# Kernel tuning notes

Measured on AMD Instinct MI355X. Metric: run time of the kernel, lower is better.

## Reference

```python
import jax, jax.numpy as jnp
import numpy as np

B, S, E, H = 2, 2048, 1024, 16
DH = E // H  # 64
FF = 4 * E


def setup_inputs() -> dict:
    key = jax.random.key(0)
    ks = jax.random.split(key, 13)
    s = 0.02
    return {
        "x": jax.random.normal(ks[0], (B, S, E), dtype=jnp.float32),
        "Wq": jax.random.normal(ks[1], (H, E, DH), dtype=jnp.float32) * s,
        "Wk": jax.random.normal(ks[2], (H, E, DH), dtype=jnp.float32) * s,
        "Wv": jax.random.normal(ks[3], (H, E, DH), dtype=jnp.float32) * s,
        "Wo": jax.random.normal(ks[4], (E, E), dtype=jnp.float32) * s,
        "bo": jnp.zeros((E,), dtype=jnp.float32),
        "W1": jax.random.normal(ks[5], (E, FF), dtype=jnp.float32) * s,
        "b1": jnp.zeros((FF,), dtype=jnp.float32),
        "W2": jax.random.normal(ks[6], (FF, E), dtype=jnp.float32) * s,
        "b2": jnp.zeros((E,), dtype=jnp.float32),
        "g1": jnp.ones((E,), dtype=jnp.float32),
        "beta1": jnp.zeros((E,), dtype=jnp.float32),
        "g2": jnp.ones((E,), dtype=jnp.float32),
        "beta2": jnp.zeros((E,), dtype=jnp.float32),
    }


def _layernorm(x, g, b, eps=1e-5):
    mu = jnp.mean(x, axis=-1, keepdims=True)
    var = jnp.var(x, axis=-1, keepdims=True)
    return (x - mu) * jax.lax.rsqrt(var + eps) * g + b


def reference(x, Wq, Wk, Wv, Wo, bo, W1, b1, W2, b2, g1, beta1, g2, beta2):
    # Pre-LN attention (dropout is identity in eval mode)
    nx = _layernorm(x, g1, beta1)
    # per-head projections, batched over heads: [B,H,S,DH]
    q = jnp.einsum('bse,hed->bhsd', nx, Wq)
    k = jnp.einsum('bse,hed->bhsd', nx, Wk)
    v = jnp.einsum('bse,hed->bhsd', nx, Wv)
    scores = jnp.einsum('bhqd,bhkd->bhqk', q, k) * (DH ** -0.5)  # [B,H,S,S]
    seq = x.shape[1]
    causal = jnp.tril(jnp.ones((seq, seq), dtype=bool))
    scores = jnp.where(causal, scores, -jnp.inf)
    w = jax.nn.softmax(scores, axis=-1)
    attn = jnp.einsum('bhqk,bhkd->bhqd', w, v)  # [B,H,S,DH]
    # concat heads (head order matches ModuleList cat order)
    attn = attn.transpose(0, 2, 1, 3).reshape(x.shape[0], seq, E)
    attn_out = attn @ Wo + bo
    x = x + attn_out
    # FFN
    nx2 = _layernorm(x, g2, beta2)
    ffn = jax.nn.relu(nx2 @ W1 + b1) @ W2 + b2
    return x + ffn
```

## Files before the change

### kernel.cpp

```cpp
#include <hip/hip_runtime.h>


typedef __attribute__((ext_vector_type(8))) short short8;
typedef __attribute__((ext_vector_type(4))) float floatx4;

__device__ inline unsigned short f32_to_bf16(float f) {
  unsigned u = __float_as_uint(f);
  unsigned rb = (u >> 16) & 1u;
  u += 0x7fffu + rb;
  return (unsigned short)(u >> 16);
}
__device__ inline unsigned f32_to_bf16_hi(float f) {
  return (__float_as_uint(f) + 0x8000u) >> 16;
}
__device__ inline float bf16_to_f32(unsigned short u) {
  return __uint_as_float(((unsigned)u) << 16);
}

__global__ __launch_bounds__(256) void transpose_to_bf16(
    const float* __restrict__ in, unsigned short* __restrict__ out,
    int R, int C, int ldo, long in_bs, long out_bs) {
  __shared__ float tile[32][33];
  in  += (size_t)blockIdx.z * in_bs;
  out += (size_t)blockIdx.z * out_bs;
  const int c0 = blockIdx.x * 32, r0 = blockIdx.y * 32;
  const int tx = threadIdx.x & 31, ty = threadIdx.x >> 5;
#pragma unroll
  for (int i = 0; i < 32; i += 8)
    tile[ty + i][tx] = in[(size_t)(r0 + ty + i) * C + c0 + tx];
  __syncthreads();
#pragma unroll
  for (int i = 0; i < 32; i += 8)
    out[(size_t)(c0 + ty + i) * ldo + r0 + tx] = f32_to_bf16(tile[tx][ty + i]);
}

__global__ __launch_bounds__(256) void transpose_v(
    const unsigned short* __restrict__ qkv, unsigned short* __restrict__ vT) {
  __shared__ unsigned short tile[32][33];
  const int bh = blockIdx.z, b = bh >> 4, h = bh & 15;
  const int k0 = blockIdx.x * 32, d0 = blockIdx.y * 32;
  const int tx = threadIdx.x & 31, ty = threadIdx.x >> 5;
#pragma unroll
  for (int i = 0; i < 32; i += 8)
    tile[ty + i][tx] = qkv[(size_t)(b * 2048 + k0 + ty + i) * 3072 + 2048 + h * 64 + d0 + tx];
  __syncthreads();
#pragma unroll
  for (int i = 0; i < 32; i += 8)
    vT[((size_t)bh * 64 + d0 + ty + i) * 2048 + k0 + tx] = tile[tx][ty + i];
}

__global__ __launch_bounds__(256) void layernorm_bf16(
    const float* __restrict__ x, const float* __restrict__ g,
    const float* __restrict__ be, unsigned short* __restrict__ out) {
  const int row = blockIdx.x;
  const int t = threadIdx.x;
  floatx4 v = ((const floatx4*)(x + (size_t)row * 1024))[t];
  float s  = v[0] + v[1] + v[2] + v[3];
  float s2 = v[0]*v[0] + v[1]*v[1] + v[2]*v[2] + v[3]*v[3];
#pragma unroll
  for (int off = 1; off < 64; off <<= 1) {
    s  += __shfl_xor(s, off);
    s2 += __shfl_xor(s2, off);
  }
  __shared__ float red[8];
  const int wave = t >> 6, lane = t & 63;
  if (lane == 0) { red[wave] = s; red[wave + 4] = s2; }
  __syncthreads();
  float ts  = red[0] + red[1] + red[2] + red[3];
  float ts2 = red[4] + red[5] + red[6] + red[7];
  float mu  = ts * (1.f / 1024.f);
  float var = ts2 * (1.f / 1024.f) - mu * mu;
  float rs  = rsqrtf(var + 1e-5f);
  floatx4 gv = ((const floatx4*)g)[t];
  floatx4 bv = ((const floatx4*)be)[t];
  ushort4 ov;
  ov.x = f32_to_bf16((v[0] - mu) * rs * gv[0] + bv[0]);
  ov.y = f32_to_bf16((v[1] - mu) * rs * gv[1] + bv[1]);
  ov.z = f32_to_bf16((v[2] - mu) * rs * gv[2] + bv[2]);
  ov.w = f32_to_bf16((v[3] - mu) * rs * gv[3] + bv[3]);
  ((ushort4*)(out + (size_t)row * 1024))[t] = ov;
}

__global__ __launch_bounds__(256, 4) void gemm_bf16(
    const unsigned short* __restrict__ A, const unsigned short* __restrict__ Bt,
    const float* __restrict__ bias, const float* __restrict__ resid,
    void* __restrict__ Cout, int M, int N, int Kfull, int Klen, int mode) {
  __shared__ unsigned short As[2][128 * 36];
  __shared__ unsigned short Bs[2][128 * 36];
  const int t = threadIdx.x;
  const int NB = gridDim.x;
  const int bid = blockIdx.y * NB + blockIdx.x;
  const int xcd = bid & 7, slot = bid >> 3;
  const int m0 = (xcd * 4 + slot / NB) * 128;
  const int n0 = (slot % NB) * 128;
  const int koff = blockIdx.z * Klen;
  const int lane = t & 63, wave = t >> 6;
  const int wm = (wave >> 1) * 64, wn = (wave & 1) * 64;
  const int l15 = lane & 15, quad = lane >> 4;

  floatx4 acc[4][4];
#pragma unroll
  for (int i = 0; i < 4; ++i)
#pragma unroll
    for (int j = 0; j < 4; ++j) acc[i][j] = floatx4{0.f, 0.f, 0.f, 0.f};

  const int srow = t >> 1;
  const int scol = (t & 1) * 16;
  const unsigned short* Ag = A + (size_t)(m0 + srow) * Kfull + koff + scol;
  const unsigned short* Bg = Bt + (size_t)(n0 + srow) * Kfull + koff + scol;
  const int sdst = srow * 36 + scol;

  uint4 pa0 = *(const uint4*)(Ag);
  uint4 pa1 = *(const uint4*)(Ag + 8);
  uint4 pb0 = *(const uint4*)(Bg);
  uint4 pb1 = *(const uint4*)(Bg + 8);

  const int KT = Klen >> 5;
  int buf = 0;
  for (int kt = 0; kt < KT; ++kt) {
    *(uint4*)&As[buf][sdst]     = pa0;
    *(uint4*)&As[buf][sdst + 8] = pa1;
    *(uint4*)&Bs[buf][sdst]     = pb0;
    *(uint4*)&Bs[buf][sdst + 8] = pb1;
    if (kt + 1 < KT) {
      const int ko = (kt + 1) * 32;
      pa0 = *(const uint4*)(Ag + ko);
      pa1 = *(const uint4*)(Ag + ko + 8);
      pb0 = *(const uint4*)(Bg + ko);
      pb1 = *(const uint4*)(Bg + ko + 8);
    }
    __syncthreads();
    short8 a[4], b[4];
#pragma unroll
    for (int i = 0; i < 4; ++i)
      a[i] = *(const short8*)&As[buf][(wm + i * 16 + l15) * 36 + quad * 8];
#pragma unroll
    for (int i = 0; i < 4; ++i)
      b[i] = *(const short8*)&Bs[buf][(wn + i * 16 + l15) * 36 + quad * 8];
#pragma unroll
    for (int i = 0; i < 4; ++i)
#pragma unroll
      for (int j = 0; j < 4; ++j)
        acc[i][j] = __builtin_amdgcn_mfma_f32_16x16x32_bf16(a[i], b[j], acc[i][j], 0, 0, 0);
    buf ^= 1;
  }

  const size_t poff = (size_t)blockIdx.z * 4096 * 1024;
#pragma unroll
  for (int i = 0; i < 4; ++i)
#pragma unroll
    for (int j = 0; j < 4; ++j) {
      const int col = n0 + wn + j * 16 + l15;
      const int rb = m0 + wm + i * 16 + quad * 4;
#pragma unroll
      for (int r = 0; r < 4; ++r) {
        const int row = rb + r;
        float v = acc[i][j][r];
        if (mode == 0) {
          ((unsigned short*)Cout)[(size_t)row * N + col] = f32_to_bf16(v);
        } else if (mode == 1) {
          v += bias[col] + resid[(size_t)row * N + col];
          ((float*)Cout)[(size_t)row * N + col] = v;
        } else if (mode == 2) {
          v += bias[col];
          v = fmaxf(v, 0.f);
          ((unsigned short*)Cout)[(size_t)row * N + col] = f32_to_bf16(v);
        } else {
          ((float*)Cout)[poff + (size_t)row * N + col] = v;
        }
      }
    }
}

__global__ __launch_bounds__(256) void splitk_reduce(
    const float* __restrict__ p, const float* __restrict__ bias,
    const float* __restrict__ resid, float* __restrict__ out) {
  const int t = threadIdx.x;
  const size_t base = (size_t)blockIdx.x * 256 + t;
  floatx4 a = ((const floatx4*)p)[base];
  floatx4 b = ((const floatx4*)p)[1048576 + base];
  floatx4 rv = ((const floatx4*)resid)[base];
  floatx4 bv = ((const floatx4*)bias)[t];
  ((floatx4*)out)[base] = a + b + rv + bv;
}

__global__ __launch_bounds__(256, 3) void flash_attn_mfma(
    const unsigned short* __restrict__ qkv,
    const unsigned short* __restrict__ vT,
    unsigned short* __restrict__ attn) {
  const int b = blockIdx.z, h = blockIdx.y, bh = b * 16 + h;
  const int qt = 15 - (int)blockIdx.x;
  const int q0 = qt * 128;
  const int t = threadIdx.x;
  const int wave = t >> 6, lane = t & 63;
  const int l15 = lane & 15, quad = lane >> 4;

  __shared__ unsigned short Ks[2][64][68];
  __shared__ unsigned short Vs[2][64][68];
  __shared__ unsigned short Ps[4][32][68];

  const size_t qbase = (size_t)b * 2048 * 3072;
  const int qrow_w = q0 + wave * 32;
  const unsigned short* Kbase = qkv + qbase + 1024 + h * 64;
  const unsigned short* Vbase = vT + (size_t)bh * 64 * 2048;

  short8 qf[2][2];
#pragma unroll
  for (int mf = 0; mf < 2; ++mf)
#pragma unroll
    for (int kc = 0; kc < 2; ++kc) {
      short8 raw = *(const short8*)(qkv + qbase +
          (size_t)(qrow_w + mf * 16 + l15) * 3072 + h * 64 + kc * 32 + quad * 8);
      short8 sc;
#pragma unroll
      for (int j = 0; j < 8; ++j)
        sc[j] = (short)f32_to_bf16(bf16_to_f32((unsigned short)raw[j]) * 0.125f);
      qf[mf][kc] = sc;
    }

  floatx4 o[2][4];
  float l_s[2] = {0.f, 0.f};
#pragma unroll
  for (int mf = 0; mf < 2; ++mf)
#pragma unroll
    for (int jd = 0; jd < 4; ++jd) o[mf][jd] = floatx4{0.f, 0.f, 0.f, 0.f};

  const int sr = t >> 3, so = (t & 7) * 8;

  uint4 kr0 = *(const uint4*)(Kbase + (size_t)sr * 3072 + so);
  uint4 kr1 = *(const uint4*)(Kbase + (size_t)(sr + 32) * 3072 + so);
  uint4 vr0 = *(const uint4*)(Vbase + (size_t)sr * 2048 + so);
  uint4 vr1 = *(const uint4*)(Vbase + (size_t)(sr + 32) * 2048 + so);

  const int ntiles = 2 * qt + 2;
  int buf = 0;
  for (int kt = 0; kt < ntiles; ++kt) {
    const int k0 = kt * 64;
    *(uint4*)&Ks[buf][sr][so]      = kr0;
    *(uint4*)&Ks[buf][sr + 32][so] = kr1;
    *(uint4*)&Vs[buf][sr][so]      = vr0;
    *(uint4*)&Vs[buf][sr + 32][so] = vr1;
    if (kt + 1 < ntiles) {
      const int k1 = k0 + 64;
      kr0 = *(const uint4*)(Kbase + (size_t)(k1 + sr) * 3072 + so);
      kr1 = *(const uint4*)(Kbase + (size_t)(k1 + sr + 32) * 3072 + so);
      vr0 = *(const uint4*)(Vbase + (size_t)sr * 2048 + k1 + so);
      vr1 = *(const uint4*)(Vbase + (size_t)(sr + 32) * 2048 + k1 + so);
    }
    __syncthreads();

    if (k0 <= qrow_w + 31) {
      short8 kf[2][4];
#pragma unroll
      for (int kc = 0; kc < 2; ++kc)
#pragma unroll
        for (int jb = 0; jb < 4; ++jb)
          kf[kc][jb] = *(const short8*)&Ks[buf][jb * 16 + l15][kc * 32 + quad * 8];

      floatx4 st[2][4];
#pragma unroll
      for (int mf = 0; mf < 2; ++mf)
#pragma unroll
        for (int jb = 0; jb < 4; ++jb) st[mf][jb] = floatx4{0.f, 0.f, 0.f, 0.f};
#pragma unroll
      for (int kc = 0; kc < 2; ++kc)
#pragma unroll
        for (int jb = 0; jb < 4; ++jb) {
#pragma unroll
          for (int mf = 0; mf < 2; ++mf)
            st[mf][jb] = __builtin_amdgcn_mfma_f32_16x16x32_bf16(
                kf[kc][jb], qf[mf][kc], st[mf][jb], 0, 0, 0);
        }

#pragma unroll
      for (int mf = 0; mf < 2; ++mf) {
        const int qq = qrow_w + mf * 16 + l15;
#pragma unroll
        for (int jb = 0; jb < 4; ++jb) {
          const int keyb = k0 + jb * 16 + quad * 4;
          float p0 = (keyb + 0 > qq) ? 0.f : __expf(st[mf][jb][0]);
          float p1 = (keyb + 1 > qq) ? 0.f : __expf(st[mf][jb][1]);
          float p2 = (keyb + 2 > qq) ? 0.f : __expf(st[mf][jb][2]);
          float p3 = (keyb + 3 > qq) ? 0.f : __expf(st[mf][jb][3]);
          l_s[mf] += (p0 + p1) + (p2 + p3);
          uint2 pk;
          pk.x = (f32_to_bf16_hi(p1) << 16) | f32_to_bf16_hi(p0);
          pk.y = (f32_to_bf16_hi(p3) << 16) | f32_to_bf16_hi(p2);
          *(uint2*)&Ps[wave][mf * 16 + l15][jb * 16 + quad * 4] = pk;
        }
      }

#pragma unroll
      for (int kc = 0; kc < 2; ++kc) {
        short8 pf0 = *(const short8*)&Ps[wave][l15][kc * 32 + quad * 8];
        short8 pf1 = *(const short8*)&Ps[wave][16 + l15][kc * 32 + quad * 8];
#pragma unroll
        for (int jd = 0; jd < 4; ++jd) {
          short8 vf = *(const short8*)&Vs[buf][jd * 16 + l15][kc * 32 + quad * 8];
          o[0][jd] = __builtin_amdgcn_mfma_f32_16x16x32_bf16(pf0, vf, o[0][jd], 0, 0, 0);
          o[1][jd] = __builtin_amdgcn_mfma_f32_16x16x32_bf16(pf1, vf, o[1][jd], 0, 0, 0);
        }
      }
    }
    buf ^= 1;
  }

#pragma unroll
  for (int mf = 0; mf < 2; ++mf) {
    l_s[mf] += __shfl_xor(l_s[mf], 16);
    l_s[mf] += __shfl_xor(l_s[mf], 32);
  }

#pragma unroll
  for (int mf = 0; mf < 2; ++mf)
#pragma unroll
    for (int r = 0; r < 4; ++r) {
      const int qloc = quad * 4 + r;
      const float lsum = __shfl(l_s[mf], qloc);
      const float rl = 1.f / lsum;
      const int row = b * 2048 + q0 + wave * 32 + mf * 16 + qloc;
#pragma unroll
      for (int jd = 0; jd < 4; ++jd)
        attn[(size_t)row * 1024 + h * 64 + jd * 16 + l15] =
            f32_to_bf16(o[mf][jd][r] * rl);
    }
}

extern "C" void kernel_launch(void* const* d_in, const int* in_sizes, int n_in,
                              void* d_out, int out_size, void* d_ws, size_t ws_size,
                              hipStream_t stream) {
  const float* x   = (const float*)d_in[0];
  const float* Wq  = (const float*)d_in[1];
  const float* Wk  = (const float*)d_in[2];
  const float* Wv  = (const float*)d_in[3];
  const float* Wo  = (const float*)d_in[4];
  const float* bo  = (const float*)d_in[5];
  const float* W1  = (const float*)d_in[6];
  const float* b1  = (const float*)d_in[7];
  const float* W2  = (const float*)d_in[8];
  const float* b2  = (const float*)d_in[9];
  const float* g1  = (const float*)d_in[10];
  const float* be1 = (const float*)d_in[11];
  const float* g2  = (const float*)d_in[12];
  const float* be2 = (const float*)d_in[13];
  float* out = (float*)d_out;

  char* ws = (char*)d_ws;
  size_t off = 0;
  auto alloc = [&](size_t bytes) -> void* {
    void* p = ws + off;
    off += (bytes + 255) & ~(size_t)255;
    return p;
  };
  unsigned short* WqkvT = (unsigned short*)alloc(3072ull * 1024 * 2);
  unsigned short* WoT   = (unsigned short*)alloc(1024ull * 1024 * 2);
  unsigned short* W1T   = (unsigned short*)alloc(4096ull * 1024 * 2);
  unsigned short* W2T   = (unsigned short*)alloc(1024ull * 4096 * 2);
  unsigned short* nx    = (unsigned short*)alloc(4096ull * 1024 * 2);
  unsigned short* qkv   = (unsigned short*)alloc(4096ull * 3072 * 2);
  unsigned short* attn  = (unsigned short*)alloc(4096ull * 1024 * 2);
  float*          x1    = (float*)alloc(4096ull * 1024 * 4);
  unsigned short* nx2   = (unsigned short*)alloc(4096ull * 1024 * 2);
  unsigned short* hbuf  = (unsigned short*)alloc(4096ull * 4096 * 2);
  unsigned short* vT    = hbuf;
  float*          part  = (float*)nx;

  dim3 blk(256);
  transpose_to_bf16<<<dim3(2, 32, 16), blk, 0, stream>>>(Wq, WqkvT, 1024, 64, 1024, 65536, 65536);
  transpose_to_bf16<<<dim3(2, 32, 16), blk, 0, stream>>>(Wk, WqkvT + 1024 * 1024, 1024, 64, 1024, 65536, 65536);
  transpose_to_bf16<<<dim3(2, 32, 16), blk, 0, stream>>>(Wv, WqkvT + 2 * 1024 * 1024, 1024, 64, 1024, 65536, 65536);
  transpose_to_bf16<<<dim3(32, 32, 1), blk, 0, stream>>>(Wo, WoT, 1024, 1024, 1024, 0, 0);
  transpose_to_bf16<<<dim3(128, 32, 1), blk, 0, stream>>>(W1, W1T, 1024, 4096, 1024, 0, 0);
  transpose_to_bf16<<<dim3(32, 128, 1), blk, 0, stream>>>(W2, W2T, 4096, 1024, 4096, 0, 0);

  layernorm_bf16<<<4096, blk, 0, stream>>>(x, g1, be1, nx);
  gemm_bf16<<<dim3(24, 32, 1), blk, 0, stream>>>(nx, WqkvT, nullptr, nullptr, qkv, 4096, 3072, 1024, 1024, 0);
  transpose_v<<<dim3(64, 2, 32), blk, 0, stream>>>(qkv, vT);
  flash_attn_mfma<<<dim3(16, 16, 2), blk, 0, stream>>>(qkv, vT, attn);
  gemm_bf16<<<dim3(8, 32, 2), blk, 0, stream>>>(attn, WoT, nullptr, nullptr, part, 4096, 1024, 1024, 512, 3);
  splitk_reduce<<<4096, blk, 0, stream>>>(part, bo, x, x1);
  layernorm_bf16<<<4096, blk, 0, stream>>>(x1, g2, be2, nx2);
  gemm_bf16<<<dim3(32, 32, 1), blk, 0, stream>>>(nx2, W1T, b1, nullptr, hbuf, 4096, 4096, 1024, 1024, 2);
  gemm_bf16<<<dim3(8, 32, 2), blk, 0, stream>>>(hbuf, W2T, nullptr, nullptr, part, 4096, 1024, 4096, 2048, 3);
  splitk_reduce<<<4096, blk, 0, stream>>>(part, b2, x1, out);
}
```

Measured before the change: 393.5 us.

## Use direct global-to-LDS loads in GEMM and fuse split-K reduce with LayerNorm

New measurement: 425.1 us. 1.08x slower.

```diff
diff --git a/kernel.cpp b/kernel.cpp
--- a/kernel.cpp
+++ b/kernel.cpp
@@ -15,6 +15,12 @@
 }
 __device__ inline float bf16_to_f32(unsigned short u) {
   return __uint_as_float(((unsigned)u) << 16);
+}
+
+__device__ inline void gload16(const void* g, void* l) {
+  __builtin_amdgcn_global_load_lds(
+      (const __attribute__((address_space(1))) void*)g,
+      (__attribute__((address_space(3))) void*)l, 16, 0, 0);
 }
 
 __global__ __launch_bounds__(256) void transpose_to_bf16(
@@ -81,12 +87,12 @@
   ((ushort4*)(out + (size_t)row * 1024))[t] = ov;
 }
 
-__global__ __launch_bounds__(256, 4) void gemm_bf16(
+__global__ __launch_bounds__(256) void gemm_bf16(
     const unsigned short* __restrict__ A, const unsigned short* __restrict__ Bt,
     const float* __restrict__ bias, const float* __restrict__ resid,
     void* __restrict__ Cout, int M, int N, int Kfull, int Klen, int mode) {
-  __shared__ unsigned short As[2][128 * 36];
-  __shared__ unsigned short Bs[2][128 * 36];
+  __shared__ unsigned short As[128 * 32];
+  __shared__ unsigned short Bs[128 * 32];
   const int t = threadIdx.x;
   const int NB = gridDim.x;
   const int bid = blockIdx.y * NB + blockIdx.x;
@@ -104,45 +110,38 @@
 #pragma unroll
     for (int j = 0; j < 4; ++j) acc[i][j] = floatx4{0.f, 0.f, 0.f, 0.f};
 
-  const int srow = t >> 1;
-  const int scol = (t & 1) * 16;
-  const unsigned short* Ag = A + (size_t)(m0 + srow) * Kfull + koff + scol;
-  const unsigned short* Bg = Bt + (size_t)(n0 + srow) * Kfull + koff + scol;
-  const int sdst = srow * 36 + scol;
-
-  uint4 pa0 = *(const uint4*)(Ag);
-  uint4 pa1 = *(const uint4*)(Ag + 8);
-  uint4 pb0 = *(const uint4*)(Bg);
-  uint4 pb1 = *(const uint4*)(Bg + 8);
+  const int srow = wave * 32 + (lane >> 2);
+  const int scol = (lane & 3) * 8;
+  const unsigned short* Ag0 = A + (size_t)(m0 + srow) * Kfull + koff + scol;
+  const unsigned short* Ag1 = Ag0 + (size_t)16 * Kfull;
+  const unsigned short* Bg0 = Bt + (size_t)(n0 + srow) * Kfull + koff + scol;
+  const unsigned short* Bg1 = Bg0 + (size_t)16 * Kfull;
+  unsigned short* lA0 = &As[(wave * 2 + 0) * 512];
+  unsigned short* lA1 = &As[(wave * 2 + 1) * 512];
+  unsigned short* lB0 = &Bs[(wave * 2 + 0) * 512];
+  unsigned short* lB1 = &Bs[(wave * 2 + 1) * 512];
 
   const int KT = Klen >> 5;
-  int buf = 0;
   for (int kt = 0; kt < KT; ++kt) {
-    *(uint4*)&As[buf][sdst]     = pa0;
-    *(uint4*)&As[buf][sdst + 8] = pa1;
-    *(uint4*)&Bs[buf][sdst]     = pb0;
-    *(uint4*)&Bs[buf][sdst + 8] = pb1;
-    if (kt + 1 < KT) {
-      const int ko = (kt + 1) * 32;
-      pa0 = *(const uint4*)(Ag + ko);
-      pa1 = *(const uint4*)(Ag + ko + 8);
-      pb0 = *(const uint4*)(Bg + ko);
-      pb1 = *(const uint4*)(Bg + ko + 8);
-    }
+    const int ko = kt * 32;
+    gload16(Ag0 + ko, lA0);
+    gload16(Ag1 + ko, lA1);
+    gload16(Bg0 + ko, lB0);
+    gload16(Bg1 + ko, lB1);
     __syncthreads();
     short8 a[4], b[4];
 #pragma unroll
     for (int i = 0; i < 4; ++i)
-      a[i] = *(const short8*)&As[buf][(wm + i * 16 + l15) * 36 + quad * 8];
+      a[i] = *(const short8*)&As[(wm + i * 16 + l15) * 32 + quad * 8];
 #pragma unroll
     for (int i = 0; i < 4; ++i)
-      b[i] = *(const short8*)&Bs[buf][(wn + i * 16 + l15) * 36 + quad * 8];
+      b[i] = *(const short8*)&Bs[(wn + i * 16 + l15) * 32 + quad * 8];
 #pragma unroll
     for (int i = 0; i < 4; ++i)
 #pragma unroll
       for (int j = 0; j < 4; ++j)
         acc[i][j] = __builtin_amdgcn_mfma_f32_16x16x32_bf16(a[i], b[j], acc[i][j], 0, 0, 0);
-    buf ^= 1;
+    __syncthreads();
   }
 
   const size_t poff = (size_t)blockIdx.z * 4096 * 1024;
@@ -182,6 +181,45 @@
   floatx4 rv = ((const floatx4*)resid)[base];
   floatx4 bv = ((const floatx4*)bias)[t];
   ((floatx4*)out)[base] = a + b + rv + bv;
+}
+
+__global__ __launch_bounds__(256) void splitk_reduce_ln(
+    const float* __restrict__ p, const float* __restrict__ bias,
+    const float* __restrict__ resid, const float* __restrict__ g,
+    const float* __restrict__ be, float* __restrict__ xout,
+    unsigned short* __restrict__ nxout) {
+  const int row = blockIdx.x, t = threadIdx.x;
+  const size_t base = (size_t)row * 256 + t;
+  floatx4 a = ((const floatx4*)p)[base];
+  floatx4 b = ((const floatx4*)p)[1048576 + base];
+  floatx4 rv = ((const floatx4*)resid)[base];
+  floatx4 bv = ((const floatx4*)bias)[t];
+  floatx4 v = a + b + rv + bv;
+  ((floatx4*)xout)[base] = v;
+  float s  = v[0] + v[1] + v[2] + v[3];
+  float s2 = v[0]*v[0] + v[1]*v[1] + v[2]*v[2] + v[3]*v[3];
+#pragma unroll
+  for (int off = 1; off < 64; off <<= 1) {
+    s  += __shfl_xor(s, off);
+    s2 += __shfl_xor(s2, off);
+  }
+  __shared__ float red[8];
+  const int wave = t >> 6, lane = t & 63;
+  if (lane == 0) { red[wave] = s; red[wave + 4] = s2; }
+  __syncthreads();
+  float ts  = red[0] + red[1] + red[2] + red[3];
+  float ts2 = red[4] + red[5] + red[6] + red[7];
+  float mu  = ts * (1.f / 1024.f);
+  float var = ts2 * (1.f / 1024.f) - mu * mu;
+  float rs  = rsqrtf(var + 1e-5f);
+  floatx4 gv = ((const floatx4*)g)[t];
+  floatx4 bev = ((const floatx4*)be)[t];
+  ushort4 ov;
+  ov.x = f32_to_bf16((v[0] - mu) * rs * gv[0] + bev[0]);
+  ov.y = f32_to_bf16((v[1] - mu) * rs * gv[1] + bev[1]);
+  ov.z = f32_to_bf16((v[2] - mu) * rs * gv[2] + bev[2]);
+  ov.w = f32_to_bf16((v[3] - mu) * rs * gv[3] + bev[3]);
+  ((ushort4*)(nxout + (size_t)row * 1024))[t] = ov;
 }
 
 __global__ __launch_bounds__(256, 3) void flash_attn_mfma(
@@ -378,8 +416,7 @@
   transpose_v<<<dim3(64, 2, 32), blk, 0, stream>>>(qkv, vT);
   flash_attn_mfma<<<dim3(16, 16, 2), blk, 0, stream>>>(qkv, vT, attn);
   gemm_bf16<<<dim3(8, 32, 2), blk, 0, stream>>>(attn, WoT, nullptr, nullptr, part, 4096, 1024, 1024, 512, 3);
-  splitk_reduce<<<4096, blk, 0, stream>>>(part, bo, x, x1);
-  layernorm_bf16<<<4096, blk, 0, stream>>>(x1, g2, be2, nx2);
+  splitk_reduce_ln<<<4096, blk, 0, stream>>>(part, bo, x, g2, be2, x1, nx2);
   gemm_bf16<<<dim3(32, 32, 1), blk, 0, stream>>>(nx2, W1T, b1, nullptr, hbuf, 4096, 4096, 1024, 1024, 2);
   gemm_bf16<<<dim3(8, 32, 2), blk, 0, stream>>>(hbuf, W2T, nullptr, nullptr, part, 4096, 1024, 4096, 2048, 3);
   splitk_reduce<<<4096, blk, 0, stream>>>(part, b2, x1, out);
```
